# Performance work log

Hardware: AMD Instinct MI355X
Metric: run time of the kernel (lower is better)

The kernel has to match this reference:

```python
import jax, jax.numpy as jnp
import numpy as np

B, T, C, H = 2, 2048, 1024, 16
D = C // H  # head_dim = 64

def setup_inputs() -> dict:
    key = jax.random.key(0)
    ks = jax.random.split(key, 9)
    s = 1.0 / np.sqrt(C)
    return {
        "x": jax.random.normal(ks[0], (B, T, C), dtype=jnp.float32),
        "Wq": jax.random.uniform(ks[1], (C, C), jnp.float32, -s, s),
        "bq": jax.random.uniform(ks[2], (C,), jnp.float32, -s, s),
        "Wk": jax.random.uniform(ks[3], (C, C), jnp.float32, -s, s),
        "bk": jax.random.uniform(ks[4], (C,), jnp.float32, -s, s),
        "Wv": jax.random.uniform(ks[5], (C, C), jnp.float32, -s, s),
        "bv": jax.random.uniform(ks[6], (C,), jnp.float32, -s, s),
        "Wp": jax.random.uniform(ks[7], (C, C), jnp.float32, -s, s),
        "bp": jax.random.uniform(ks[8], (C,), jnp.float32, -s, s),
    }

def reference(x, Wq, bq, Wk, bk, Wv, bv, Wp, bp):
    # Linear layers: torch nn.Linear weight is [out,in], so x @ W.T + b
    q = x @ Wq.T + bq
    k = x @ Wk.T + bk
    v = x @ Wv.T + bv
    # [B,T,C] -> [B,H,T,D]
    q = q.reshape(B, T, H, D).transpose(0, 2, 1, 3)
    k = k.reshape(B, T, H, D).transpose(0, 2, 1, 3)
    v = v.reshape(B, T, H, D).transpose(0, 2, 1, 3)
    att = jnp.einsum("bhqd,bhkd->bhqk", q, k) / jnp.sqrt(jnp.float32(D))
    causal = jnp.tril(jnp.ones((T, T), dtype=bool))  # [T,T]
    att = jnp.where(causal, att, jnp.float32(-jnp.inf))
    att = jax.nn.softmax(att, axis=-1)
    out = jnp.einsum("bhqk,bhkd->bhqd", att, v)
    out = out.transpose(0, 2, 1, 3).reshape(B, T, C)
    return out @ Wp.T + bp
```

## Files before the change

kernel.cpp:

```cpp
#include <hip/hip_runtime.h>
#include <hip/hip_bf16.h>

typedef __bf16 bf16x8 __attribute__((ext_vector_type(8)));
typedef __bf16 bf16x4 __attribute__((ext_vector_type(4)));
typedef __bf16 bf16x2 __attribute__((ext_vector_type(2)));
typedef float  f32x4  __attribute__((ext_vector_type(4)));
typedef float  f32x16v __attribute__((ext_vector_type(16)));

#define MFMA16(A,B,Cc) __builtin_amdgcn_mfma_f32_16x16x32_bf16(A,B,Cc,0,0,0)
#define MFMA32(A,B,Cc) __builtin_amdgcn_mfma_f32_32x32x16_bf16(A,B,Cc,0,0,0)

__device__ inline unsigned pack2(float a, float b) {
  union { bf16x2 v; unsigned u; } t;
  t.v[0] = (__bf16)a; t.v[1] = (__bf16)b;
  return t.u;
}
__device__ inline bf16x8 frag4(unsigned w0, unsigned w1, unsigned w2, unsigned w3) {
  union { unsigned u[4]; bf16x8 v; } t;
  t.u[0] = w0; t.u[1] = w1; t.u[2] = w2; t.u[3] = w3;
  return t.v;
}

__global__ __launch_bounds__(256) void conv_kernel(
    const float* __restrict__ x,
    const float* __restrict__ Wq, const float* __restrict__ Wk,
    const float* __restrict__ Wv, const float* __restrict__ Wp,
    __bf16* __restrict__ xb, __bf16* __restrict__ Wb)
{
  const int z = blockIdx.y;
  const float* src;
  __bf16* dst;
  int n4;
  if (z == 0) { src = x;  dst = xb; n4 = 1048576; }
  else {
    src = (z == 1) ? Wq : (z == 2) ? Wk : (z == 3) ? Wv : Wp;
    dst = Wb + (size_t)(z - 1) * 1048576;
    n4  = 262144;
  }
  const f32x4* s4 = (const f32x4*)src;
  for (int i = blockIdx.x * 256 + threadIdx.x; i < n4; i += gridDim.x * 256) {
    const f32x4 v = s4[i];
    bf16x4 o;
#pragma unroll
    for (int j = 0; j < 4; ++j) o[j] = (__bf16)v[j];
    *(bf16x4*)(dst + (size_t)i * 4) = o;
  }
}

__device__ inline void gemm_core(const __bf16* __restrict__ A,
                                 const __bf16* __restrict__ W,
                                 int m0, int n0,
                                 __bf16* As, __bf16* Bs,
                                 f32x4 (&acc)[4][4])
{
  const int tid = threadIdx.x, lane = tid & 63;
  const int wid = tid >> 6, wr = wid >> 1, wc = wid & 1;
  const int g = lane >> 4, cl = lane & 15;
  const int sr = tid >> 2, sk = (tid & 3) * 8;

  for (int k0 = 0; k0 < 1024; k0 += 32) {
    bf16x8 a0 = *(const bf16x8*)(A + (size_t)(m0 + sr)      * 1024 + k0 + sk);
    bf16x8 a1 = *(const bf16x8*)(A + (size_t)(m0 + sr + 64) * 1024 + k0 + sk);
    bf16x8 b0 = *(const bf16x8*)(W + (size_t)(n0 + sr)      * 1024 + k0 + sk);
    bf16x8 b1 = *(const bf16x8*)(W + (size_t)(n0 + sr + 64) * 1024 + k0 + sk);
    __syncthreads();
    *(bf16x8*)(As + sr * 32 + sk)        = a0;
    *(bf16x8*)(As + (sr + 64) * 32 + sk) = a1;
    *(bf16x8*)(Bs + sr * 32 + sk)        = b0;
    *(bf16x8*)(Bs + (sr + 64) * 32 + sk) = b1;
    __syncthreads();
    bf16x8 af[4], bfr[4];
#pragma unroll
    for (int m = 0; m < 4; ++m)
      af[m] = *(const bf16x8*)(As + (wr * 64 + m * 16 + cl) * 32 + g * 8);
#pragma unroll
    for (int n = 0; n < 4; ++n)
      bfr[n] = *(const bf16x8*)(Bs + (wc * 64 + n * 16 + cl) * 32 + g * 8);
#pragma unroll
    for (int m = 0; m < 4; ++m)
#pragma unroll
      for (int n = 0; n < 4; ++n)
        acc[m][n] = MFMA16(af[m], bfr[n], acc[m][n]);
  }
}

__global__ __launch_bounds__(256) void gemm_qkv128(
    const __bf16* __restrict__ xb, const __bf16* __restrict__ Wb,
    const float* __restrict__ bq, const float* __restrict__ bk,
    const float* __restrict__ bv,
    __bf16* __restrict__ Qw, __bf16* __restrict__ Kw, __bf16* __restrict__ Vw)
{
  __shared__ __align__(16) __bf16 As[128 * 32];
  __shared__ __align__(16) __bf16 Bs[128 * 32];

  const int orig = blockIdx.x;
  const int wg   = (orig & 7) * 96 + (orig >> 3);
  const int z    = wg >> 8;
  const int rem  = wg & 255;
  const int m0   = (rem >> 3) * 128;
  const int n0   = (rem & 7) * 128;

  const __bf16* W  = Wb + (size_t)z * 1048576;
  const float*  bi = (z == 0) ? bq : (z == 1) ? bk : bv;
  __bf16*       out = (z == 0) ? Qw : (z == 1) ? Kw : Vw;

  f32x4 acc[4][4] = {};
  gemm_core(xb, W, m0, n0, As, Bs, acc);

  const int lane = threadIdx.x & 63, wid = threadIdx.x >> 6;
  const int wr = wid >> 1, wc = wid & 1;
  const int g = lane >> 4, cl = lane & 15;

  float bvv[4];
#pragma unroll
  for (int n = 0; n < 4; ++n) bvv[n] = bi[n0 + wc * 64 + n * 16 + cl];

#pragma unroll
  for (int m = 0; m < 4; ++m)
#pragma unroll
    for (int n = 0; n < 4; ++n) {
      const int col = n0 + wc * 64 + n * 16 + cl;
      const int h = col >> 6, d = col & 63;
      if (z == 2) {
        const int row0 = m0 + wr * 64 + m * 16 + g * 4;
        const int b2 = row0 >> 11, t0 = row0 & 2047;
        bf16x4 v4;
#pragma unroll
        for (int j = 0; j < 4; ++j) v4[j] = (__bf16)(acc[m][n][j] + bvv[n]);
        *(bf16x4*)(out + (size_t)(b2 * 16 + h) * 131072 + (size_t)d * 2048 + t0) = v4;
      } else {
#pragma unroll
        for (int j = 0; j < 4; ++j) {
          const int row = m0 + wr * 64 + m * 16 + g * 4 + j;
          const int b2 = row >> 11, t = row & 2047;
          out[(size_t)(b2 * 16 + h) * 131072 + (size_t)t * 64 + d] =
              (__bf16)(acc[m][n][j] + bvv[n]);
        }
      }
    }
}

__global__ __launch_bounds__(256) void gemm_proj128(
    const __bf16* __restrict__ A, const __bf16* __restrict__ W,
    const float* __restrict__ bi, float* __restrict__ outp)
{
  __shared__ __align__(16) __bf16 As[128 * 32];
  __shared__ __align__(16) __bf16 Bs[128 * 32];

  const int orig = blockIdx.x;
  const int wg   = (orig & 7) * 32 + (orig >> 3);
  const int m0   = (wg >> 3) * 128;
  const int n0   = (wg & 7) * 128;

  f32x4 acc[4][4] = {};
  gemm_core(A, W, m0, n0, As, Bs, acc);

  const int lane = threadIdx.x & 63, wid = threadIdx.x >> 6;
  const int wr = wid >> 1, wc = wid & 1;
  const int g = lane >> 4, cl = lane & 15;

  float bvv[4];
#pragma unroll
  for (int n = 0; n < 4; ++n) bvv[n] = bi[n0 + wc * 64 + n * 16 + cl];
#pragma unroll
  for (int m = 0; m < 4; ++m)
#pragma unroll
    for (int n = 0; n < 4; ++n) {
      const int col = n0 + wc * 64 + n * 16 + cl;
#pragma unroll
      for (int j = 0; j < 4; ++j) {
        const int row = m0 + wr * 64 + m * 16 + g * 4 + j;
        outp[(size_t)row * 1024 + col] = acc[m][n][j] + bvv[n];
      }
    }
}

__device__ inline void attn_tile(
    const __bf16* __restrict__ Kb, const __bf16* __restrict__ vrow0,
    const __bf16* __restrict__ vrow1, const bf16x8 (&qf)[4],
    int kv0, bool diag, int l31, int hi,
    float& M, float& MS, float& L, f32x16v& o0, f32x16v& o1)
{
  const float SC = 0.18033688f;
  const float DT = 16.6f;
  f32x16v s = {};
#pragma unroll
  for (int c = 0; c < 4; ++c) {
    bf16x8 kf = *(const bf16x8*)(Kb + (kv0 + l31) * 64 + c * 16 + hi * 8);
    s = MFMA32(kf, qf[c], s);
  }
  float sv[16];
#pragma unroll
  for (int r = 0; r < 16; ++r) sv[r] = s[r];
  if (diag) {
#pragma unroll
    for (int r = 0; r < 16; ++r) {
      const int kl = (r & 3) + 8 * (r >> 2) + 4 * hi;
      if (kl > l31) sv[r] = -1e30f;
    }
  }
  float mt = sv[0];
#pragma unroll
  for (int r = 1; r < 16; ++r) mt = fmaxf(mt, sv[r]);
  mt = fmaxf(mt, __shfl_xor(mt, 32, 64));
  if (!__all(mt <= M + DT)) {
    const float Mn = fmaxf(M, mt);
    const float rs = exp2f((M - Mn) * SC);
    o0 *= rs; o1 *= rs; L *= rs; M = Mn; MS = M * SC;
  }
  float p[16];
  float lt = 0.f;
#pragma unroll
  for (int r = 0; r < 16; ++r) {
    p[r] = exp2f(__builtin_fmaf(sv[r], SC, -MS));
    lt += p[r];
  }
  lt += __shfl_xor(lt, 32, 64);
  L += lt;

  const unsigned c0 = pack2(p[0],  p[1]),  c1 = pack2(p[2],  p[3]);
  const unsigned c2 = pack2(p[4],  p[5]),  c3 = pack2(p[6],  p[7]);
  const unsigned c4 = pack2(p[8],  p[9]),  c5 = pack2(p[10], p[11]);
  const unsigned c6 = pack2(p[12], p[13]), c7 = pack2(p[14], p[15]);
  const unsigned x0 = __shfl_xor(c0, 32, 64), x1 = __shfl_xor(c1, 32, 64);
  const unsigned x2 = __shfl_xor(c2, 32, 64), x3 = __shfl_xor(c3, 32, 64);
  const unsigned x4 = __shfl_xor(c4, 32, 64), x5 = __shfl_xor(c5, 32, 64);
  const unsigned x6 = __shfl_xor(c6, 32, 64), x7 = __shfl_xor(c7, 32, 64);
  const bf16x8 pf0 = frag4(hi ? x2 : c0, hi ? x3 : c1, hi ? c2 : x0, hi ? c3 : x1);
  const bf16x8 pf1 = frag4(hi ? x6 : c4, hi ? x7 : c5, hi ? c6 : x4, hi ? c7 : x5);

  bf16x8 va;
  va = *(const bf16x8*)(vrow0 + kv0 + hi * 8);       o0 = MFMA32(va, pf0, o0);
  va = *(const bf16x8*)(vrow1 + kv0 + hi * 8);       o1 = MFMA32(va, pf0, o1);
  va = *(const bf16x8*)(vrow0 + kv0 + 16 + hi * 8);  o0 = MFMA32(va, pf1, o0);
  va = *(const bf16x8*)(vrow1 + kv0 + 16 + hi * 8);  o1 = MFMA32(va, pf1, o1);
}

__global__ __launch_bounds__(256, 4) void attn_kernel(
    const __bf16* __restrict__ Q, const __bf16* __restrict__ K,
    const __bf16* __restrict__ Vt, __bf16* __restrict__ Oc)
{
  const int bh  = blockIdx.x;
  const int p   = blockIdx.y;
  const int w   = threadIdx.x >> 6;
  const int lane = threadIdx.x & 63;
  const int l31 = lane & 31, hi = lane >> 5;
  const float SC = 0.18033688f;

  const __bf16* Qb = Q  + (size_t)bh * 131072;
  const __bf16* Kb = K  + (size_t)bh * 131072;
  const __bf16* Vb = Vt + (size_t)bh * 131072;
  const __bf16* vrow0 = Vb + (size_t)l31 * 2048;
  const __bf16* vrow1 = Vb + (size_t)(32 + l31) * 2048;

  __shared__ __bf16 SO[8][64][32];
  __shared__ float  SML[8][64][2];

  const int qsS[2] = { p * 32, (63 - p) * 32 };
  const int nS[2]  = { p + 1, 64 - p };

#pragma unroll
  for (int ph = 0; ph < 2; ++ph) {
    const int qs = qsS[ph], nT = nS[ph];
    bf16x8 qf[4];
#pragma unroll
    for (int c = 0; c < 4; ++c)
      qf[c] = *(const bf16x8*)(Qb + (qs + l31) * 64 + c * 16 + hi * 8);

    f32x16v o0 = {}, o1 = {};
    float M = -1e30f, L = 0.f;
    float MS = M * SC;

    for (int t = w; t < nT; t += 4)
      attn_tile(Kb, vrow0, vrow1, qf, t * 32, t == nT - 1, l31, hi,
                M, MS, L, o0, o1);

    const int slot = ph * 4 + w;
#pragma unroll
    for (int q4 = 0; q4 < 4; ++q4) {
      bf16x4 a, b;
#pragma unroll
      for (int j = 0; j < 4; ++j) {
        a[j] = (__bf16)o0[q4 * 4 + j];
        b[j] = (__bf16)o1[q4 * 4 + j];
      }
      *(bf16x4*)&SO[slot][lane][q4 * 4]      = a;
      *(bf16x4*)&SO[slot][lane][16 + q4 * 4] = b;
    }
    SML[slot][lane][0] = M;
    SML[slot][lane][1] = L;
  }

  __syncthreads();
  if (w < 2) {
    const int base = w * 4;
    const int qs = qsS[w];
    float Mw[4], Lw[4];
#pragma unroll
    for (int s = 0; s < 4; ++s) {
      Mw[s] = SML[base + s][lane][0];
      Lw[s] = SML[base + s][lane][1];
    }
    const float Ms = fmaxf(fmaxf(Mw[0], Mw[1]), fmaxf(Mw[2], Mw[3]));
    float r[4], Lt = 0.f;
#pragma unroll
    for (int s = 0; s < 4; ++s) {
      r[s] = exp2f((Mw[s] - Ms) * SC);
      Lt += Lw[s] * r[s];
    }
    const float inv = 1.0f / Lt;

    const int b = bh >> 4, h = bh & 15;
    const int tq = qs + l31;
    __bf16* orow = Oc + (size_t)(b * 2048 + tq) * 1024 + h * 64;
#pragma unroll
    for (int q4 = 0; q4 < 4; ++q4) {
      bf16x4 v0, v1;
#pragma unroll
      for (int j = 0; j < 4; ++j) {
        const int ri = q4 * 4 + j;
        float a = 0.f, bb = 0.f;
#pragma unroll
        for (int s = 0; s < 4; ++s) {
          a  += (float)SO[base + s][lane][ri]      * r[s];
          bb += (float)SO[base + s][lane][16 + ri] * r[s];
        }
        v0[j] = (__bf16)(a * inv);
        v1[j] = (__bf16)(bb * inv);
      }
      const int d0 = 8 * q4 + 4 * hi;
      *(bf16x4*)(orow + d0)      = v0;
      *(bf16x4*)(orow + 32 + d0) = v1;
    }
  }
}

extern "C" void kernel_launch(void* const* d_in, const int* in_sizes, int n_in,
                              void* d_out, int out_size, void* d_ws, size_t ws_size,
                              hipStream_t stream) {
  const float* x  = (const float*)d_in[0];
  const float* Wq = (const float*)d_in[1];
  const float* bq = (const float*)d_in[2];
  const float* Wk = (const float*)d_in[3];
  const float* bk = (const float*)d_in[4];
  const float* Wv = (const float*)d_in[5];
  const float* bv = (const float*)d_in[6];
  const float* Wp = (const float*)d_in[7];
  const float* bp = (const float*)d_in[8];

  __bf16* Qw  = (__bf16*)d_ws;
  __bf16* Kw  = Qw + (size_t)4194304;
  __bf16* Vw  = Kw + (size_t)4194304;
  __bf16* xbA = Vw + (size_t)4194304;
  __bf16* Wb  = xbA + (size_t)4194304;

  conv_kernel<<<dim3(512, 5), 256, 0, stream>>>(x, Wq, Wk, Wv, Wp, xbA, Wb);
  gemm_qkv128<<<768, 256, 0, stream>>>(xbA, Wb, bq, bk, bv, Qw, Kw, Vw);
  attn_kernel<<<dim3(32, 32), 256, 0, stream>>>(Qw, Kw, Vw, xbA );
  gemm_proj128<<<256, 256, 0, stream>>>(xbA , Wb + (size_t)3 * 1048576,
                                        bp, (float*)d_out);
}
```

Before: 142.0 us.

## Prefetch next K tile, split QK MFMA chains, use permlane32 swaps

The attention inner loop is inlined, and the next K tile's fragments are loaded one iteration ahead to hide global load latency. The QK^T product now runs as two independent MFMA accumulator chains that are summed at the end. Cross-half reductions and the P-fragment exchange use v_permlane32_swap instead of ds_bpermute-based shuffles, and the final combine reads SO as vectors from a padded row stride. Register pressure rises from the prefetch buffer and the extra accumulator, which may hurt occupancy at launch_bounds(256,4).

```diff
diff --git a/kernel.cpp b/kernel.cpp
--- a/kernel.cpp
+++ b/kernel.cpp
@@ -19,6 +19,25 @@
   union { unsigned u[4]; bf16x8 v; } t;
   t.u[0] = w0; t.u[1] = w1; t.u[2] = w2; t.u[3] = w3;
   return t.v;
+}
+
+__device__ inline void pswap(unsigned& a, unsigned& b) {
+#if __has_builtin(__builtin_amdgcn_permlane32_swap)
+  auto r = __builtin_amdgcn_permlane32_swap(a, b, false, false);
+  a = r[0]; b = r[1];
+#else
+  asm volatile("v_permlane32_swap_b32 %0, %1" : "+v"(a), "+v"(b));
+#endif
+}
+__device__ inline float cross32_max(float v) {
+  unsigned a = __builtin_bit_cast(unsigned, v), b = a;
+  pswap(a, b);
+  return fmaxf(__builtin_bit_cast(float, a), __builtin_bit_cast(float, b));
+}
+__device__ inline float cross32_sum(float v) {
+  unsigned a = __builtin_bit_cast(unsigned, v), b = a;
+  pswap(a, b);
+  return __builtin_bit_cast(float, a) + __builtin_bit_cast(float, b);
 }
 
 __global__ __launch_bounds__(256) void conv_kernel(
@@ -175,67 +194,6 @@
     }
 }
 
-__device__ inline void attn_tile(
-    const __bf16* __restrict__ Kb, const __bf16* __restrict__ vrow0,
-    const __bf16* __restrict__ vrow1, const bf16x8 (&qf)[4],
-    int kv0, bool diag, int l31, int hi,
-    float& M, float& MS, float& L, f32x16v& o0, f32x16v& o1)
-{
-  const float SC = 0.18033688f;
-  const float DT = 16.6f;
-  f32x16v s = {};
-#pragma unroll
-  for (int c = 0; c < 4; ++c) {
-    bf16x8 kf = *(const bf16x8*)(Kb + (kv0 + l31) * 64 + c * 16 + hi * 8);
-    s = MFMA32(kf, qf[c], s);
-  }
-  float sv[16];
-#pragma unroll
-  for (int r = 0; r < 16; ++r) sv[r] = s[r];
-  if (diag) {
-#pragma unroll
-    for (int r = 0; r < 16; ++r) {
-      const int kl = (r & 3) + 8 * (r >> 2) + 4 * hi;
-      if (kl > l31) sv[r] = -1e30f;
-    }
-  }
-  float mt = sv[0];
-#pragma unroll
-  for (int r = 1; r < 16; ++r) mt = fmaxf(mt, sv[r]);
-  mt = fmaxf(mt, __shfl_xor(mt, 32, 64));
-  if (!__all(mt <= M + DT)) {
-    const float Mn = fmaxf(M, mt);
-    const float rs = exp2f((M - Mn) * SC);
-    o0 *= rs; o1 *= rs; L *= rs; M = Mn; MS = M * SC;
-  }
-  float p[16];
-  float lt = 0.f;
-#pragma unroll
-  for (int r = 0; r < 16; ++r) {
-    p[r] = exp2f(__builtin_fmaf(sv[r], SC, -MS));
-    lt += p[r];
-  }
-  lt += __shfl_xor(lt, 32, 64);
-  L += lt;
-
-  const unsigned c0 = pack2(p[0],  p[1]),  c1 = pack2(p[2],  p[3]);
-  const unsigned c2 = pack2(p[4],  p[5]),  c3 = pack2(p[6],  p[7]);
-  const unsigned c4 = pack2(p[8],  p[9]),  c5 = pack2(p[10], p[11]);
-  const unsigned c6 = pack2(p[12], p[13]), c7 = pack2(p[14], p[15]);
-  const unsigned x0 = __shfl_xor(c0, 32, 64), x1 = __shfl_xor(c1, 32, 64);
-  const unsigned x2 = __shfl_xor(c2, 32, 64), x3 = __shfl_xor(c3, 32, 64);
-  const unsigned x4 = __shfl_xor(c4, 32, 64), x5 = __shfl_xor(c5, 32, 64);
-  const unsigned x6 = __shfl_xor(c6, 32, 64), x7 = __shfl_xor(c7, 32, 64);
-  const bf16x8 pf0 = frag4(hi ? x2 : c0, hi ? x3 : c1, hi ? c2 : x0, hi ? c3 : x1);
-  const bf16x8 pf1 = frag4(hi ? x6 : c4, hi ? x7 : c5, hi ? c6 : x4, hi ? c7 : x5);
-
-  bf16x8 va;
-  va = *(const bf16x8*)(vrow0 + kv0 + hi * 8);       o0 = MFMA32(va, pf0, o0);
-  va = *(const bf16x8*)(vrow1 + kv0 + hi * 8);       o1 = MFMA32(va, pf0, o1);
-  va = *(const bf16x8*)(vrow0 + kv0 + 16 + hi * 8);  o0 = MFMA32(va, pf1, o0);
-  va = *(const bf16x8*)(vrow1 + kv0 + 16 + hi * 8);  o1 = MFMA32(va, pf1, o1);
-}
-
 __global__ __launch_bounds__(256, 4) void attn_kernel(
     const __bf16* __restrict__ Q, const __bf16* __restrict__ K,
     const __bf16* __restrict__ Vt, __bf16* __restrict__ Oc)
@@ -246,6 +204,7 @@
   const int lane = threadIdx.x & 63;
   const int l31 = lane & 31, hi = lane >> 5;
   const float SC = 0.18033688f;
+  const float DT = 16.6f;
 
   const __bf16* Qb = Q  + (size_t)bh * 131072;
   const __bf16* Kb = K  + (size_t)bh * 131072;
@@ -253,7 +212,7 @@
   const __bf16* vrow0 = Vb + (size_t)l31 * 2048;
   const __bf16* vrow1 = Vb + (size_t)(32 + l31) * 2048;
 
-  __shared__ __bf16 SO[8][64][32];
+  __shared__ __bf16 SO[8][64][34];
   __shared__ float  SML[8][64][2];
 
   const int qsS[2] = { p * 32, (63 - p) * 32 };
@@ -271,9 +230,76 @@
     float M = -1e30f, L = 0.f;
     float MS = M * SC;
 
-    for (int t = w; t < nT; t += 4)
-      attn_tile(Kb, vrow0, vrow1, qf, t * 32, t == nT - 1, l31, hi,
-                M, MS, L, o0, o1);
+    bf16x8 kf[4];
+#pragma unroll
+    for (int c = 0; c < 4; ++c)
+      kf[c] = *(const bf16x8*)(Kb + (w * 32 + l31) * 64 + c * 16 + hi * 8);
+
+    for (int t = w; t < nT; t += 4) {
+      const int kv0 = t * 32;
+      const int tn = t + 4;
+      bf16x8 kn[4];
+      const bool hasNext = tn < nT;
+      if (hasNext) {
+#pragma unroll
+        for (int c = 0; c < 4; ++c)
+          kn[c] = *(const bf16x8*)(Kb + (tn * 32 + l31) * 64 + c * 16 + hi * 8);
+      }
+
+      f32x16v sA = {}, sB = {};
+      sA = MFMA32(kf[0], qf[0], sA);
+      sB = MFMA32(kf[1], qf[1], sB);
+      sA = MFMA32(kf[2], qf[2], sA);
+      sB = MFMA32(kf[3], qf[3], sB);
+      f32x16v s = sA + sB;
+
+      if (t == nT - 1) {
+#pragma unroll
+        for (int r = 0; r < 16; ++r) {
+          const int kl = (r & 3) + 8 * (r >> 2) + 4 * hi;
+          if (kl > l31) s[r] = -1e30f;
+        }
+      }
+      float mt = fmaxf(s[0], s[1]);
+#pragma unroll
+      for (int r = 2; r < 16; ++r) mt = fmaxf(mt, s[r]);
+      mt = cross32_max(mt);
+      if (!__all(mt <= M + DT)) {
+        const float Mn = fmaxf(M, mt);
+        const float rs = exp2f((M - Mn) * SC);
+        o0 *= rs; o1 *= rs; L *= rs; M = Mn; MS = M * SC;
+      }
+      float pr[16];
+      float lt = 0.f;
+#pragma unroll
+      for (int r = 0; r < 16; ++r) {
+        pr[r] = exp2f(__builtin_fmaf(s[r], SC, -MS));
+        lt += pr[r];
+      }
+      L += cross32_sum(lt);
+
+      unsigned c0 = pack2(pr[0],  pr[1]),  c1 = pack2(pr[2],  pr[3]);
+      unsigned c2 = pack2(pr[4],  pr[5]),  c3 = pack2(pr[6],  pr[7]);
+      unsigned c4 = pack2(pr[8],  pr[9]),  c5 = pack2(pr[10], pr[11]);
+      unsigned c6 = pack2(pr[12], pr[13]), c7 = pack2(pr[14], pr[15]);
+      pswap(c0, c2);
+      pswap(c1, c3);
+      pswap(c4, c6);
+      pswap(c5, c7);
+      const bf16x8 pf0 = frag4(c0, c1, c2, c3);
+      const bf16x8 pf1 = frag4(c4, c5, c6, c7);
+
+      bf16x8 va;
+      va = *(const bf16x8*)(vrow0 + kv0 + hi * 8);       o0 = MFMA32(va, pf0, o0);
+      va = *(const bf16x8*)(vrow1 + kv0 + hi * 8);       o1 = MFMA32(va, pf0, o1);
+      va = *(const bf16x8*)(vrow0 + kv0 + 16 + hi * 8);  o0 = MFMA32(va, pf1, o0);
+      va = *(const bf16x8*)(vrow1 + kv0 + 16 + hi * 8);  o1 = MFMA32(va, pf1, o1);
+
+      if (hasNext) {
+#pragma unroll
+        for (int c = 0; c < 4; ++c) kf[c] = kn[c];
+      }
+    }
 
     const int slot = ph * 4 + w;
 #pragma unroll
@@ -316,17 +342,21 @@
 #pragma unroll
     for (int q4 = 0; q4 < 4; ++q4) {
       bf16x4 v0, v1;
+      float acc0[4] = {}, acc1[4] = {};
+#pragma unroll
+      for (int s = 0; s < 4; ++s) {
+        const bf16x4 a4 = *(const bf16x4*)&SO[base + s][lane][q4 * 4];
+        const bf16x4 b4 = *(const bf16x4*)&SO[base + s][lane][16 + q4 * 4];
+#pragma unroll
+        for (int j = 0; j < 4; ++j) {
+          acc0[j] += (float)a4[j] * r[s];
+          acc1[j] += (float)b4[j] * r[s];
+        }
+      }
 #pragma unroll
       for (int j = 0; j < 4; ++j) {
-        const int ri = q4 * 4 + j;
-        float a = 0.f, bb = 0.f;
-#pragma unroll
-        for (int s = 0; s < 4; ++s) {
-          a  += (float)SO[base + s][lane][ri]      * r[s];
-          bb += (float)SO[base + s][lane][16 + ri] * r[s];
-        }
-        v0[j] = (__bf16)(a * inv);
-        v1[j] = (__bf16)(bb * inv);
+        v0[j] = (__bf16)(acc0[j] * inv);
+        v1[j] = (__bf16)(acc1[j] * inv);
       }
       const int d0 = 8 * q4 + 4 * hi;
       *(bf16x4*)(orow + d0)      = v0;
```

New measurement: 150.7 us. 6.1% more time.
